# Performance work log

Hardware: AMD Instinct MI355X
Metric: run time of the kernel (lower is better)

Reference implementation:

```python
import jax, jax.numpy as jnp
import numpy as np

B, S, E, H = 2, 2048, 1024, 16
D = E // H  # head_dim = 64


def setup_inputs() -> dict:
    key = jax.random.key(0)
    k1, k2, k3 = jax.random.split(key, 3)
    scale = 0.02  # GPT-2 init scale
    return {
        "hidden_states": jax.random.normal(k1, (B, S, E), dtype=jnp.float32),
        "c_attn_w": jax.random.normal(k2, (E, 3 * E), dtype=jnp.float32) * scale,
        "c_attn_b": jnp.zeros((3 * E,), dtype=jnp.float32),
        "c_proj_w": jax.random.normal(k3, (E, E), dtype=jnp.float32) * scale,
        "c_proj_b": jnp.zeros((E,), dtype=jnp.float32),
    }


def reference(hidden_states, c_attn_w, c_attn_b, c_proj_w, c_proj_b):
    # Conv1D: x @ W + b  -> qkv [B, S, 3E]
    qkv = hidden_states @ c_attn_w + c_attn_b
    q, k, v = jnp.split(qkv, 3, axis=-1)

    # split heads -> [B, H, S, D]
    def split_heads(t):
        return t.reshape(B, S, H, D).transpose(0, 2, 1, 3)

    q, k, v = split_heads(q), split_heads(k), split_heads(v)

    # naive full attention: QK^T / sqrt(D) -> softmax -> @ V
    attn_weights = jnp.einsum("bhqd,bhkd->bhqk", q, k) / jnp.sqrt(
        jnp.asarray(D, dtype=q.dtype)
    )
    attn_weights = jax.nn.softmax(attn_weights, axis=-1)
    attn_output = jnp.einsum("bhqk,bhkd->bhqd", attn_weights, v)

    # merge heads -> [B, S, E], then output projection
    attn_output = attn_output.transpose(0, 2, 1, 3).reshape(B, S, E)
    attn_output = attn_output @ c_proj_w + c_proj_b
    return attn_output
```

## Files before the change

kernel.cpp:

```cpp
#include <hip/hip_runtime.h>

#define SEQ 2048
#define EMB 1024
#define KDIM 1024
#define CF 0.180336880111113f

typedef __attribute__((ext_vector_type(8))) short short8_t;
typedef __attribute__((ext_vector_type(4))) float floatx4;
typedef __attribute__((ext_vector_type(4))) unsigned short ushort4_t;

#define GLOAD16(gp, lp)                                                        \
  __builtin_amdgcn_global_load_lds(                                            \
      (const __attribute__((address_space(1))) void*)(gp),                     \
      (__attribute__((address_space(3))) void*)(lp), 16, 0, 0)

#define WGBAR()                                   \
  do {                                            \
    __asm__ __volatile__("" ::: "memory");        \
    __builtin_amdgcn_s_barrier();                 \
    __asm__ __volatile__("" ::: "memory");        \
  } while (0)

static __device__ __forceinline__ unsigned short f2bf(float x) {
  unsigned int u = __float_as_uint(x);
  return (unsigned short)((u + 0x7fffu + ((u >> 16) & 1u)) >> 16);
}

__global__ __launch_bounds__(256) void conv_bf(
    const float* __restrict__ X, unsigned short* __restrict__ Y, int n4) {
  int i = blockIdx.x * 256 + threadIdx.x;
  if (i >= n4) return;
  float4 v = *(const float4*)&X[(size_t)i * 4];
  ushort4_t h = {f2bf(v.x), f2bf(v.y), f2bf(v.z), f2bf(v.w)};
  *(ushort4_t*)&Y[(size_t)i * 4] = h;
}

__global__ __launch_bounds__(256) void tconv(
    const float* __restrict__ W, unsigned short* __restrict__ T, int N, int K) {
  __shared__ float Tl[64][65];
  const int tid = threadIdx.x, lx = tid & 15, ly = tid >> 4;
  const int n0 = blockIdx.x * 64, k0 = blockIdx.y * 64;
#pragma unroll
  for (int u = 0; u < 4; ++u) {
    int r = u * 16 + ly;
    float4 v = *(const float4*)&W[(size_t)(k0 + r) * N + n0 + lx * 4];
    Tl[r][lx * 4 + 0] = v.x;
    Tl[r][lx * 4 + 1] = v.y;
    Tl[r][lx * 4 + 2] = v.z;
    Tl[r][lx * 4 + 3] = v.w;
  }
  __syncthreads();
#pragma unroll
  for (int u = 0; u < 4; ++u) {
    int n = u * 16 + ly;
    ushort4_t h;
#pragma unroll
    for (int v = 0; v < 4; ++v) h[v] = f2bf(Tl[lx * 4 + v][n]);
    *(ushort4_t*)&T[(size_t)(n0 + n) * K + k0 + lx * 4] = h;
  }
}

template <int MODE, int BN>
__global__ __launch_bounds__(256) void gemm_bf(
    const unsigned short* __restrict__ Ag, const unsigned short* __restrict__ Bg,
    const float* __restrict__ bias, float* __restrict__ outF,
    unsigned short* __restrict__ qk, unsigned short* __restrict__ vt, int N) {
  __shared__ __attribute__((aligned(16))) unsigned short Ah[128 * 64];
  __shared__ __attribute__((aligned(16))) unsigned short Bh[BN * 64];
  const int NJ = BN / 32;

  const int tid = threadIdx.x;
  const int w = tid >> 6, lane = tid & 63;
  const int quad = lane >> 4, c = lane & 15;
  const int bm = blockIdx.y * 128, bn = blockIdx.x * BN;
  const int wm = (w >> 1) * 64, wn = (w & 1) * (BN / 2);

  const unsigned short* gsrc = (w < 2) ? Ag : Bg;
  unsigned short* ldst = (w < 2) ? (Ah + (w & 1) * 64 * 64) : (Bh + (w & 1) * (BN / 2) * 64);
  const int rbase = (w < 2) ? (bm + (w & 1) * 64) : (bn + (w & 1) * (BN / 2));
  const int nloads = (w < 2) ? 8 : (BN / 16);
  const int srow = lane >> 3;
  const int sblk = (lane & 7) ^ srow;
  const char* gp0 = (const char*)(gsrc + (size_t)(rbase + srow) * KDIM) + sblk * 16;

  floatx4 acc[4][NJ];
  const floatx4 z = {0.f, 0.f, 0.f, 0.f};
#pragma unroll
  for (int i = 0; i < 4; ++i)
#pragma unroll
    for (int j = 0; j < NJ; ++j) acc[i][j] = z;

  const int rk = c & 7;

  for (int k0 = 0; k0 < KDIM; k0 += 64) {
    __syncthreads();
    const char* gp = gp0 + k0 * 2;
    for (int i = 0; i < nloads; ++i) GLOAD16(gp + (size_t)i * 8 * (KDIM * 2), &ldst[i * 512]);
    __syncthreads();

#pragma unroll
    for (int kq = 0; kq < 2; ++kq) {
      const int oct = ((4 * kq + quad) ^ rk) * 8;
      short8_t a[4], b[NJ];
#pragma unroll
      for (int i = 0; i < 4; ++i)
        a[i] = *(const short8_t*)&Ah[(wm + 16 * i + c) * 64 + oct];
#pragma unroll
      for (int j = 0; j < NJ; ++j)
        b[j] = *(const short8_t*)&Bh[(wn + 16 * j + c) * 64 + oct];
#pragma unroll
      for (int i = 0; i < 4; ++i)
#pragma unroll
        for (int j = 0; j < NJ; ++j)
          acc[i][j] = __builtin_amdgcn_mfma_f32_16x16x32_bf16(a[i], b[j], acc[i][j], 0, 0, 0);
    }
  }

#pragma unroll
  for (int i = 0; i < 4; ++i) {
    const int r0 = bm + wm + 16 * i + quad * 4;
#pragma unroll
    for (int j = 0; j < NJ; ++j) {
      const int col = bn + wn + 16 * j + c;
      const float bv = bias[col];
      float v0 = acc[i][j][0] + bv, v1 = acc[i][j][1] + bv;
      float v2 = acc[i][j][2] + bv, v3 = acc[i][j][3] + bv;
      if (MODE == 0) {
        if (col < 1024) { v0 *= CF; v1 *= CF; v2 *= CF; v3 *= CF; }
        if (bn < 2048) {
          qk[(size_t)(r0 + 0) * 2048 + col] = f2bf(v0);
          qk[(size_t)(r0 + 1) * 2048 + col] = f2bf(v1);
          qk[(size_t)(r0 + 2) * 2048 + col] = f2bf(v2);
          qk[(size_t)(r0 + 3) * 2048 + col] = f2bf(v3);
        } else {
          const int c2 = col - 2048, hh = c2 >> 6, d = c2 & 63;
          const int bb = r0 >> 11, s = r0 & 2047;
          ushort4_t pk = {f2bf(v0), f2bf(v1), f2bf(v2), f2bf(v3)};
          *(ushort4_t*)&vt[((size_t)(bb * 16 + hh) * 64 + d) * 2048 + s] = pk;
        }
      } else {
        outF[(size_t)(r0 + 0) * N + col] = v0;
        outF[(size_t)(r0 + 1) * N + col] = v1;
        outF[(size_t)(r0 + 2) * N + col] = v2;
        outF[(size_t)(r0 + 3) * N + col] = v3;
      }
    }
  }
}

static __device__ __forceinline__ void stage_kv(
    int w, int srow, int sblkg, const unsigned short* __restrict__ gK,
    const unsigned short* __restrict__ gV, unsigned short* Kbuf,
    unsigned short* Vbuf, int jt) {
  if (w < 2) {
    const unsigned short* g0 = gK + (size_t)(jt * 64 + w * 32 + srow) * 2048 + sblkg * 8;
    unsigned short* l0 = &Kbuf[(w * 32) * 64];
#pragma unroll
    for (int i = 0; i < 4; ++i) GLOAD16(g0 + (size_t)i * 8 * 2048, &l0[i * 512]);
  } else {
    const unsigned short* g0 = gV + (size_t)((w - 2) * 32 + srow) * 2048 + jt * 64 + sblkg * 8;
    unsigned short* l0 = &Vbuf[((w - 2) * 32) * 64];
#pragma unroll
    for (int i = 0; i < 4; ++i) GLOAD16(g0 + (size_t)i * 8 * 2048, &l0[i * 512]);
  }
}

__global__ __launch_bounds__(256) void attn4(
    const unsigned short* __restrict__ qk, const unsigned short* __restrict__ vt,
    unsigned short* __restrict__ ao) {
  __shared__ __attribute__((aligned(16))) unsigned short Ks[2][64 * 64];
  __shared__ __attribute__((aligned(16))) unsigned short Vs[2][64 * 64];
  __shared__ __attribute__((aligned(16))) unsigned short Ps[4][32 * 64];

  const int tid = threadIdx.x;
  const int w = tid >> 6, lane = tid & 63, quad = lane >> 4, c = lane & 15;
  const int q0 = blockIdx.x * 128, h = blockIdx.y, b = blockIdx.z;
  const int rk = c & 7;

  short8_t qf[2][2];
  {
    const size_t rb = (size_t)b * SEQ + q0 + w * 32;
#pragma unroll
    for (int mi = 0; mi < 2; ++mi) {
      const size_t qr = (rb + mi * 16 + c) * 2048 + h * 64 + quad * 8;
      qf[mi][0] = *(const short8_t*)&qk[qr];
      qf[mi][1] = *(const short8_t*)&qk[qr + 32];
    }
  }
  __asm__ __volatile__("s_waitcnt vmcnt(0)" ::: "memory");

  floatx4 O[2][4], Osum[2];
  const floatx4 z = {0.f, 0.f, 0.f, 0.f};
#pragma unroll
  for (int mi = 0; mi < 2; ++mi) {
    Osum[mi] = z;
#pragma unroll
    for (int dg = 0; dg < 4; ++dg) O[mi][dg] = z;
  }
  short8_t ones;
#pragma unroll
  for (int e = 0; e < 8; ++e) ones[e] = (short)0x3F80;

  const int srow = lane >> 3;
  const int sblkg = (lane & 7) ^ srow;
  const unsigned short* gK = qk + (size_t)b * SEQ * 2048 + 1024 + h * 64;
  const unsigned short* gV = vt + (size_t)(b * 16 + h) * 64 * 2048;
  unsigned short* myPs = Ps[w];

  stage_kv(w, srow, sblkg, gK, gV, Ks[0], Vs[0], 0);

  for (int t = 0; t < 32; ++t) {
    const int cur = t & 1;
    WGBAR();
    stage_kv(w, srow, sblkg, gK, gV, Ks[cur ^ 1], Vs[cur ^ 1], (t + 1) & 31);
    __asm__ __volatile__("s_waitcnt vmcnt(4)" ::: "memory");
    WGBAR();
    const unsigned short* Kc = Ks[cur];
    const unsigned short* Vc = Vs[cur];

    floatx4 S[2][4];
#pragma unroll
    for (int mi = 0; mi < 2; ++mi)
#pragma unroll
      for (int jg = 0; jg < 4; ++jg) S[mi][jg] = z;
#pragma unroll
    for (int kd = 0; kd < 2; ++kd) {
      const int oct = ((4 * kd + quad) ^ rk) * 8;
#pragma unroll
      for (int jg = 0; jg < 4; ++jg) {
        short8_t kf = *(const short8_t*)&Kc[(jg * 16 + c) * 64 + oct];
#pragma unroll
        for (int mi = 0; mi < 2; ++mi)
          S[mi][jg] = __builtin_amdgcn_mfma_f32_16x16x32_bf16(kf, qf[mi][kd], S[mi][jg], 0, 0, 0);
      }
    }

#pragma unroll
    for (int mi = 0; mi < 2; ++mi) {
      const int qrow = (mi * 16 + c) * 64;
#pragma unroll
      for (int jg = 0; jg < 4; ++jg) {
        float p0 = __builtin_amdgcn_exp2f(S[mi][jg][0]);
        float p1 = __builtin_amdgcn_exp2f(S[mi][jg][1]);
        float p2 = __builtin_amdgcn_exp2f(S[mi][jg][2]);
        float p3 = __builtin_amdgcn_exp2f(S[mi][jg][3]);
        unsigned int pk01 = (__float_as_uint(p1) & 0xFFFF0000u) | (__float_as_uint(p0) >> 16);
        unsigned int pk23 = (__float_as_uint(p3) & 0xFFFF0000u) | (__float_as_uint(p2) >> 16);
        const int jp0 = 8 * jg + 2 * quad;
#pragma unroll
        for (int u = 0; u < 2; ++u) {
          const int jp = jp0 + u;
          const int off = ((jp >> 2) ^ rk) * 8 + (jp & 3) * 2;
          *(unsigned int*)&myPs[qrow + off] = u ? pk23 : pk01;
        }
      }
    }
    __asm__ __volatile__("s_waitcnt lgkmcnt(0)" ::: "memory");

#pragma unroll
    for (int kq = 0; kq < 2; ++kq) {
      const int oct = ((4 * kq + quad) ^ rk) * 8;
      short8_t pb[2];
#pragma unroll
      for (int mi = 0; mi < 2; ++mi) {
        pb[mi] = *(const short8_t*)&myPs[(mi * 16 + c) * 64 + oct];
        Osum[mi] = __builtin_amdgcn_mfma_f32_16x16x32_bf16(ones, pb[mi], Osum[mi], 0, 0, 0);
      }
#pragma unroll
      for (int dg = 0; dg < 4; ++dg) {
        short8_t vf = *(const short8_t*)&Vc[(dg * 16 + c) * 64 + oct];
#pragma unroll
        for (int mi = 0; mi < 2; ++mi)
          O[mi][dg] = __builtin_amdgcn_mfma_f32_16x16x32_bf16(vf, pb[mi], O[mi][dg], 0, 0, 0);
      }
    }
  }

  __asm__ __volatile__("s_waitcnt vmcnt(0)" ::: "memory");

#pragma unroll
  for (int mi = 0; mi < 2; ++mi) {
    const float inv = 1.0f / Osum[mi][0];
    const size_t row = (size_t)b * SEQ + q0 + w * 32 + mi * 16 + c;
#pragma unroll
    for (int dg = 0; dg < 4; ++dg) {
      ushort4_t ov = {f2bf(O[mi][dg][0] * inv), f2bf(O[mi][dg][1] * inv),
                      f2bf(O[mi][dg][2] * inv), f2bf(O[mi][dg][3] * inv)};
      *(ushort4_t*)&ao[row * EMB + h * 64 + dg * 16 + quad * 4] = ov;
    }
  }
}

extern "C" void kernel_launch(void* const* d_in, const int* in_sizes, int n_in,
                              void* d_out, int out_size, void* d_ws, size_t ws_size,
                              hipStream_t stream) {
  const float* hs = (const float*)d_in[0];
  const float* c_attn_w = (const float*)d_in[1];
  const float* c_attn_b = (const float*)d_in[2];
  const float* c_proj_w = (const float*)d_in[3];
  const float* c_proj_b = (const float*)d_in[4];
  float* out = (float*)d_out;

  char* ws = (char*)d_ws;
  unsigned short* hsb = (unsigned short*)(ws + 0);
  unsigned short* qk  = (unsigned short*)(ws + 8388608);
  unsigned short* vt  = (unsigned short*)(ws + 25165824);
  unsigned short* aob = (unsigned short*)(ws + 33554432);
  unsigned short* w1t = (unsigned short*)(ws + 41943040);
  unsigned short* w2t = (unsigned short*)(ws + 48234496);

  conv_bf<<<4096, 256, 0, stream>>>(hs, hsb, (2 * SEQ * EMB) / 4);
  tconv<<<dim3(48, 16), 256, 0, stream>>>(c_attn_w, w1t, 3 * EMB, EMB);
  tconv<<<dim3(16, 16), 256, 0, stream>>>(c_proj_w, w2t, EMB, EMB);
  gemm_bf<0, 128><<<dim3(24, 32), 256, 0, stream>>>(hsb, w1t, c_attn_b, nullptr, qk, vt, 3 * EMB);
  attn4<<<dim3(16, 16, 2), 256, 0, stream>>>(qk, vt, aob);
  gemm_bf<1, 64><<<dim3(16, 32), 256, 0, stream>>>(aob, w2t, c_proj_b, out, nullptr, nullptr, EMB);
}
```

Baseline: 197.6 us.

## Merge prep kernels, triple-buffer attention KV, and vectorize GEMM epilogue stores

Folds the three conversion/transpose launches into one prep kernel to cut launch overhead. The GEMM MFMA operand order is swapped so each lane holds four consecutive columns, which allows vectorized bias loads and row-contiguous stores for qk and the fp32 output; the V-transpose store becomes four scalar strided writes. The attention kernel moves from a double to a triple KV buffer, prefetching two tiles ahead and removing one barrier per iteration, at the cost of more LDS. The s_waitcnt vmcnt(4) count was kept even though two stages are now in flight, and the final GEMM is instantiated with MODE=2, which the epilogue routes to the fp32 output branch.

```diff
diff --git a/kernel.cpp b/kernel.cpp
--- a/kernel.cpp
+++ b/kernel.cpp
@@ -26,20 +26,11 @@
   return (unsigned short)((u + 0x7fffu + ((u >> 16) & 1u)) >> 16);
 }
 
-__global__ __launch_bounds__(256) void conv_bf(
-    const float* __restrict__ X, unsigned short* __restrict__ Y, int n4) {
-  int i = blockIdx.x * 256 + threadIdx.x;
-  if (i >= n4) return;
-  float4 v = *(const float4*)&X[(size_t)i * 4];
-  ushort4_t h = {f2bf(v.x), f2bf(v.y), f2bf(v.z), f2bf(v.w)};
-  *(ushort4_t*)&Y[(size_t)i * 4] = h;
-}
-
-__global__ __launch_bounds__(256) void tconv(
-    const float* __restrict__ W, unsigned short* __restrict__ T, int N, int K) {
+static __device__ __forceinline__ void tconv_tile(
+    const float* __restrict__ W, unsigned short* __restrict__ T, int N, int K,
+    int n0, int k0, int tid) {
   __shared__ float Tl[64][65];
-  const int tid = threadIdx.x, lx = tid & 15, ly = tid >> 4;
-  const int n0 = blockIdx.x * 64, k0 = blockIdx.y * 64;
+  const int lx = tid & 15, ly = tid >> 4;
 #pragma unroll
   for (int u = 0; u < 4; ++u) {
     int r = u * 16 + ly;
@@ -60,11 +51,30 @@
   }
 }
 
+__global__ __launch_bounds__(256) void prep(
+    const float* __restrict__ hs, const float* __restrict__ caw,
+    const float* __restrict__ cpw, unsigned short* __restrict__ hsb,
+    unsigned short* __restrict__ w1t, unsigned short* __restrict__ w2t) {
+  const int bid = blockIdx.x, tid = threadIdx.x;
+  if (bid < 4096) {
+    const int i = bid * 256 + tid;
+    float4 v = *(const float4*)&hs[(size_t)i * 4];
+    ushort4_t h = {f2bf(v.x), f2bf(v.y), f2bf(v.z), f2bf(v.w)};
+    *(ushort4_t*)&hsb[(size_t)i * 4] = h;
+  } else if (bid < 4864) {
+    const int idx = bid - 4096;
+    tconv_tile(caw, w1t, 3 * EMB, EMB, (idx % 48) * 64, (idx / 48) * 64, tid);
+  } else {
+    const int idx = bid - 4864;
+    tconv_tile(cpw, w2t, EMB, EMB, (idx % 16) * 64, (idx / 16) * 64, tid);
+  }
+}
+
 template <int MODE, int BN>
 __global__ __launch_bounds__(256) void gemm_bf(
     const unsigned short* __restrict__ Ag, const unsigned short* __restrict__ Bg,
     const float* __restrict__ bias, float* __restrict__ outF,
-    unsigned short* __restrict__ qk, unsigned short* __restrict__ vt, int N) {
+    unsigned short* __restrict__ qk, unsigned short* __restrict__ vt) {
   __shared__ __attribute__((aligned(16))) unsigned short Ah[128 * 64];
   __shared__ __attribute__((aligned(16))) unsigned short Bh[BN * 64];
   const int NJ = BN / 32;
@@ -112,37 +122,33 @@
       for (int i = 0; i < 4; ++i)
 #pragma unroll
         for (int j = 0; j < NJ; ++j)
-          acc[i][j] = __builtin_amdgcn_mfma_f32_16x16x32_bf16(a[i], b[j], acc[i][j], 0, 0, 0);
+          acc[i][j] = __builtin_amdgcn_mfma_f32_16x16x32_bf16(b[j], a[i], acc[i][j], 0, 0, 0);
     }
   }
 
 #pragma unroll
   for (int i = 0; i < 4; ++i) {
-    const int r0 = bm + wm + 16 * i + quad * 4;
+    const int row = bm + wm + 16 * i + c;
 #pragma unroll
     for (int j = 0; j < NJ; ++j) {
-      const int col = bn + wn + 16 * j + c;
-      const float bv = bias[col];
-      float v0 = acc[i][j][0] + bv, v1 = acc[i][j][1] + bv;
-      float v2 = acc[i][j][2] + bv, v3 = acc[i][j][3] + bv;
+      const int col0 = bn + wn + 16 * j + quad * 4;
+      floatx4 v = acc[i][j] + *(const floatx4*)&bias[col0];
       if (MODE == 0) {
-        if (col < 1024) { v0 *= CF; v1 *= CF; v2 *= CF; v3 *= CF; }
-        if (bn < 2048) {
-          qk[(size_t)(r0 + 0) * 2048 + col] = f2bf(v0);
-          qk[(size_t)(r0 + 1) * 2048 + col] = f2bf(v1);
-          qk[(size_t)(r0 + 2) * 2048 + col] = f2bf(v2);
-          qk[(size_t)(r0 + 3) * 2048 + col] = f2bf(v3);
+        if (col0 < 1024) v = v * CF;
+        if (col0 < 2048) {
+          ushort4_t pk = {f2bf(v[0]), f2bf(v[1]), f2bf(v[2]), f2bf(v[3])};
+          *(ushort4_t*)&qk[(size_t)row * 2048 + col0] = pk;
         } else {
-          const int c2 = col - 2048, hh = c2 >> 6, d = c2 & 63;
-          const int bb = r0 >> 11, s = r0 & 2047;
-          ushort4_t pk = {f2bf(v0), f2bf(v1), f2bf(v2), f2bf(v3)};
-          *(ushort4_t*)&vt[((size_t)(bb * 16 + hh) * 64 + d) * 2048 + s] = pk;
+          const int c2 = col0 - 2048, hh = c2 >> 6, d0 = c2 & 63;
+          const int bb = row >> 11, s = row & 2047;
+          unsigned short* vb = &vt[((size_t)(bb * 16 + hh) * 64 + d0) * 2048 + s];
+          vb[0 * 2048] = f2bf(v[0]);
+          vb[1 * 2048] = f2bf(v[1]);
+          vb[2 * 2048] = f2bf(v[2]);
+          vb[3 * 2048] = f2bf(v[3]);
         }
       } else {
-        outF[(size_t)(r0 + 0) * N + col] = v0;
-        outF[(size_t)(r0 + 1) * N + col] = v1;
-        outF[(size_t)(r0 + 2) * N + col] = v2;
-        outF[(size_t)(r0 + 3) * N + col] = v3;
+        *(floatx4*)&outF[(size_t)row * 1024 + col0] = v;
       }
     }
   }
@@ -165,11 +171,11 @@
   }
 }
 
-__global__ __launch_bounds__(256) void attn4(
+__global__ __launch_bounds__(256) void attn6(
     const unsigned short* __restrict__ qk, const unsigned short* __restrict__ vt,
     unsigned short* __restrict__ ao) {
-  __shared__ __attribute__((aligned(16))) unsigned short Ks[2][64 * 64];
-  __shared__ __attribute__((aligned(16))) unsigned short Vs[2][64 * 64];
+  __shared__ __attribute__((aligned(16))) unsigned short Ks[3][64 * 64];
+  __shared__ __attribute__((aligned(16))) unsigned short Vs[3][64 * 64];
   __shared__ __attribute__((aligned(16))) unsigned short Ps[4][32 * 64];
 
   const int tid = threadIdx.x;
@@ -208,15 +214,14 @@
   unsigned short* myPs = Ps[w];
 
   stage_kv(w, srow, sblkg, gK, gV, Ks[0], Vs[0], 0);
+  stage_kv(w, srow, sblkg, gK, gV, Ks[1], Vs[1], 1);
 
   for (int t = 0; t < 32; ++t) {
-    const int cur = t & 1;
-    WGBAR();
-    stage_kv(w, srow, sblkg, gK, gV, Ks[cur ^ 1], Vs[cur ^ 1], (t + 1) & 31);
     __asm__ __volatile__("s_waitcnt vmcnt(4)" ::: "memory");
     WGBAR();
-    const unsigned short* Kc = Ks[cur];
-    const unsigned short* Vc = Vs[cur];
+    stage_kv(w, srow, sblkg, gK, gV, Ks[(t + 2) % 3], Vs[(t + 2) % 3], (t + 2) & 31);
+    const unsigned short* Kc = Ks[t % 3];
+    const unsigned short* Vc = Vs[t % 3];
 
     floatx4 S[2][4];
 #pragma unroll
@@ -309,10 +314,8 @@
   unsigned short* w1t = (unsigned short*)(ws + 41943040);
   unsigned short* w2t = (unsigned short*)(ws + 48234496);
 
-  conv_bf<<<4096, 256, 0, stream>>>(hs, hsb, (2 * SEQ * EMB) / 4);
-  tconv<<<dim3(48, 16), 256, 0, stream>>>(c_attn_w, w1t, 3 * EMB, EMB);
-  tconv<<<dim3(16, 16), 256, 0, stream>>>(c_proj_w, w2t, EMB, EMB);
-  gemm_bf<0, 128><<<dim3(24, 32), 256, 0, stream>>>(hsb, w1t, c_attn_b, nullptr, qk, vt, 3 * EMB);
-  attn4<<<dim3(16, 16, 2), 256, 0, stream>>>(qk, vt, aob);
-  gemm_bf<1, 64><<<dim3(16, 32), 256, 0, stream>>>(aob, w2t, c_proj_b, out, nullptr, nullptr, EMB);
-}
+  prep<<<5120, 256, 0, stream>>>(hs, c_attn_w, c_proj_w, hsb, w1t, w2t);
+  gemm_bf<0, 128><<<dim3(24, 32), 256, 0, stream>>>(hsb, w1t, c_attn_b, nullptr, qk, vt);
+  attn6<<<dim3(16, 16, 2), 256, 0, stream>>>(qk, vt, aob);
+  gemm_bf<2, 64><<<dim3(16, 32), 256, 0, stream>>>(aob, w2t, c_proj_b, out, nullptr, nullptr);
+}
```

Measured after the change: 193.4 us. 1.02x faster.
